# Kernel optimization log

Measured on AMD Instinct MI355X. Metric: run time of the kernel, lower is better.

## Reference

```python
import jax, jax.numpy as jnp
import numpy as np

N, DIM = 100000, 512
HID = DIM // 2


def _mlp(z, W1, b1, W2, b2):
    # shared scorer: [N, dim] -> [N, 1]
    h = jax.nn.relu(z @ W1 + b1)
    return h @ W2 + b2


def setup_inputs() -> dict:
    key = jax.random.key(0)
    k1, k2, k3, k4 = jax.random.split(key, 4)
    s1 = 1.0 / np.sqrt(DIM)
    s2 = 1.0 / np.sqrt(HID)
    return {
        "z1": jax.random.normal(k1, (N, DIM), dtype=jnp.float32),
        "z2": jax.random.normal(k2, (N, DIM), dtype=jnp.float32),
        "W1": jax.random.normal(k3, (DIM, HID), dtype=jnp.float32) * s1,
        "b1": jnp.zeros((HID,), dtype=jnp.float32),
        "W2": jax.random.normal(k4, (HID, 1), dtype=jnp.float32) * s2,
        "b2": jnp.zeros((1,), dtype=jnp.float32),
    }


def reference(z1, z2, W1, b1, W2, b2):
    x = _mlp(z1, W1, b1, W2, b2)  # [N, 1]
    y = _mlp(z2, W1, b1, W2, b2)  # [N, 1]
    # exp-normalize pair: score_x = e^x / (e^x + e^y) == sigmoid(x - y)
    # computed exactly as in the original (plain exp, no max-subtract)
    e_x = jnp.exp(x)
    e_y = jnp.exp(y)
    denom = e_x + e_y
    score_x = e_x / denom  # [N, 1]
    score_y = e_y / denom  # [N, 1]
    # diag(score) @ z  ==  score * z  (row-wise broadcast scale)
    return score_x * z1 + score_y * z2
```

## Files before the change

### kernel.cpp

```cpp
#include <hip/hip_runtime.h>
#include <hip/hip_bf16.h>
#include <cmath>

#define DIM 512
#define HID 256
#define ROWS_PB 32
#define NCHUNK 16
#define CB 16384

typedef __attribute__((ext_vector_type(8))) short short8;
typedef __attribute__((ext_vector_type(4))) float f32x4;

__device__ __forceinline__ unsigned short f2bf(float f) {
  union { float f; unsigned u; } v; v.f = f;
  unsigned u = v.u;
  return (unsigned short)((u + 0x7FFFu + ((u >> 16) & 1u)) >> 16);
}

__global__ void w1_swz_kernel(const float* __restrict__ W1,
                              unsigned short* __restrict__ w1s) {
  int tid = blockIdx.x * blockDim.x + threadIdx.x;
  if (tid >= DIM * HID) return;
  int k = tid / HID;
  int c = tid - k * HID;
  w1s[(((k >> 3) * HID) + c) * 8 + (k & 7)] = f2bf(W1[tid]);
}

__device__ __forceinline__ short8 cvt8(const f32x4 p0, const f32x4 p1) {
  short8 r;
  r[0] = (short)f2bf(p0[0]); r[1] = (short)f2bf(p0[1]);
  r[2] = (short)f2bf(p0[2]); r[3] = (short)f2bf(p0[3]);
  r[4] = (short)f2bf(p1[0]); r[5] = (short)f2bf(p1[1]);
  r[6] = (short)f2bf(p1[2]); r[7] = (short)f2bf(p1[3]);
  return r;
}

__global__ __launch_bounds__(256, 4) void fa_main_kernel(
    const float* __restrict__ z1, const float* __restrict__ z2,
    const unsigned short* __restrict__ w1s,
    const float* __restrict__ b1, const float* __restrict__ W2,
    const float* __restrict__ b2, float* __restrict__ out, int n) {
  __shared__ unsigned short Bs[2][CB / 2];
  __shared__ float xs[2][ROWS_PB];

  const int t = threadIdx.x;
  const int w = t >> 6;
  const int l = t & 63;
  const int l15 = l & 15, l16 = l >> 4;
  const int src = w & 1;
  const int tile = w >> 1;
  const int row0 = blockIdx.x * ROWS_PB;
  if (row0 >= n) return;
  const int myrow = row0 + tile * 16 + l15;
  const bool rok = myrow < n;
  const float* zz = src ? z2 : z1;
  const float* ap = zz + (size_t)myrow * DIM + (l16 << 3);
  const f32x4 zf4 = (f32x4){0.f, 0.f, 0.f, 0.f};

  {
    const char* gsrc = (const char*)w1s + l * 16;
#pragma unroll
    for (int r = w; r < 16; r += 4)
      __builtin_amdgcn_global_load_lds(
          (const __attribute__((address_space(1))) void*)(gsrc + r * 1024),
          (__attribute__((address_space(3))) void*)((char*)&Bs[0][0] + r * 1024),
          16, 0, 0);
  }
  f32x4 pa0 = rok ? *(const f32x4*)(ap) : zf4;
  f32x4 pa1 = rok ? *(const f32x4*)(ap + 4) : zf4;

  f32x4 acc[16];
#pragma unroll
  for (int f = 0; f < 16; ++f) acc[f] = zf4;

  __syncthreads();

  for (int c = 0; c < NCHUNK; ++c) {
    const int cur = c & 1;
    f32x4 na0 = zf4, na1 = zf4;
    if (c + 1 < NCHUNK) {
      const char* gsrc = (const char*)w1s + (c + 1) * CB + l * 16;
#pragma unroll
      for (int r = w; r < 16; r += 4)
        __builtin_amdgcn_global_load_lds(
            (const __attribute__((address_space(1))) void*)(gsrc + r * 1024),
            (__attribute__((address_space(3))) void*)((char*)&Bs[cur ^ 1][0] +
                                                      r * 1024),
            16, 0, 0);
      const float* apn = ap + ((c + 1) << 5);
      na0 = rok ? *(const f32x4*)(apn) : zf4;
      na1 = rok ? *(const f32x4*)(apn + 4) : zf4;
    }
    const short8 af = cvt8(pa0, pa1);
    const short8* bp = (const short8*)&Bs[cur][0] + (l16 << 8) + l15;
#pragma unroll
    for (int f = 0; f < 16; ++f) {
      const short8 bf = bp[f << 4];
      acc[f] = __builtin_amdgcn_mfma_f32_16x16x32_bf16(af, bf, acc[f], 0, 0, 0);
    }
    pa0 = na0;
    pa1 = na1;
    __syncthreads();
  }

  float part[4] = {0.f, 0.f, 0.f, 0.f};
#pragma unroll
  for (int f = 0; f < 16; ++f) {
    const int cc = (f << 4) + l15;
    const float w2v = W2[cc];
    const float b1v = b1[cc];
#pragma unroll
    for (int r = 0; r < 4; ++r) {
      const float h = acc[f][r] + b1v;
      part[r] += (h > 0.f) ? h * w2v : 0.f;
    }
  }
#pragma unroll
  for (int r = 0; r < 4; ++r) {
#pragma unroll
    for (int m = 1; m < 16; m <<= 1) part[r] += __shfl_xor(part[r], m, 16);
  }
  if (l15 == 0) {
#pragma unroll
    for (int r = 0; r < 4; ++r)
      xs[src][tile * 16 + (l16 << 2) + r] = part[r];
  }
  __syncthreads();

  const int colh = src << 8;
#pragma unroll 1
  for (int r = 0; r < 16; ++r) {
    const int rl = tile * 16 + r;
    const int grow = row0 + rl;
    if (grow < n) {
      const float d = xs[1][rl] - xs[0][rl];
      const float sx = 1.f / (1.f + __expf(d));
      const float sy = 1.f - sx;
      const size_t off = (size_t)grow * DIM + colh + (l << 2);
      const f32x4 a4 = *(const f32x4*)(z1 + off);
      const f32x4 b4 = *(const f32x4*)(z2 + off);
      f32x4 o;
      o[0] = sx * a4[0] + sy * b4[0];
      o[1] = sx * a4[1] + sy * b4[1];
      o[2] = sx * a4[2] + sy * b4[2];
      o[3] = sx * a4[3] + sy * b4[3];
      *(f32x4*)(out + off) = o;
    }
  }
}

extern "C" void kernel_launch(void* const* d_in, const int* in_sizes, int n_in,
                              void* d_out, int out_size, void* d_ws,
                              size_t ws_size, hipStream_t stream) {
  const float* z1 = (const float*)d_in[0];
  const float* z2 = (const float*)d_in[1];
  const float* W1 = (const float*)d_in[2];
  const float* b1 = (const float*)d_in[3];
  const float* W2 = (const float*)d_in[4];
  const float* b2 = (const float*)d_in[5];
  float* out = (float*)d_out;
  const int n = in_sizes[0] / DIM;
  unsigned short* w1s = (unsigned short*)d_ws;

  hipLaunchKernelGGL(w1_swz_kernel, dim3((DIM * HID + 255) / 256), dim3(256),
                     0, stream, W1, w1s);
  const int nwg = (n + ROWS_PB - 1) / ROWS_PB;
  hipLaunchKernelGGL(fa_main_kernel, dim3(nwg), dim3(256), 0, stream, z1, z2,
                     w1s, b1, W2, b2, out, n);
}
```

Baseline: 211.8 us.

## Deepen A-prefetch and replace per-chunk syncthreads with explicit vmcnt waits

Restructures the K-chunk loop so W1 staging into LDS is issued after a single barrier per iteration. The barrier is guarded by a hand-written s_waitcnt vmcnt that waits only for the current chunk's LDS loads. A-operand register prefetch now runs two chunks ahead using a double-buffered register array. The loop is fully unrolled and fenced with sched_barriers. The aim is to hide more global-load latency and drop the trailing __syncthreads, at the cost of more registers and a dependence on exact memory-op counts.

```diff
diff --git a/kernel.cpp b/kernel.cpp
--- a/kernel.cpp
+++ b/kernel.cpp
@@ -50,57 +50,61 @@
   const int src = w & 1;
   const int tile = w >> 1;
   const int row0 = blockIdx.x * ROWS_PB;
-  if (row0 >= n) return;
   const int myrow = row0 + tile * 16 + l15;
   const bool rok = myrow < n;
   const float* zz = src ? z2 : z1;
   const float* ap = zz + (size_t)myrow * DIM + (l16 << 3);
   const f32x4 zf4 = (f32x4){0.f, 0.f, 0.f, 0.f};
 
-  {
-    const char* gsrc = (const char*)w1s + l * 16;
+  auto STAGE = [&](int cc) {
+    const char* gsrc = (const char*)w1s + cc * CB + l * 16;
+    char* ldst = (char*)&Bs[cc & 1][0];
 #pragma unroll
-    for (int r = w; r < 16; r += 4)
+    for (int r = 0; r < 4; ++r) {
+      const int rr = w + r * 4;
       __builtin_amdgcn_global_load_lds(
-          (const __attribute__((address_space(1))) void*)(gsrc + r * 1024),
-          (__attribute__((address_space(3))) void*)((char*)&Bs[0][0] + r * 1024),
-          16, 0, 0);
-  }
-  f32x4 pa0 = rok ? *(const f32x4*)(ap) : zf4;
-  f32x4 pa1 = rok ? *(const f32x4*)(ap + 4) : zf4;
+          (const __attribute__((address_space(1))) void*)(gsrc + rr * 1024),
+          (__attribute__((address_space(3))) void*)(ldst + rr * 1024), 16, 0,
+          0);
+    }
+  };
+
+  f32x4 pa[2][2];
+  STAGE(0);
+  __builtin_amdgcn_sched_barrier(0);
+  pa[0][0] = rok ? *(const f32x4*)(ap) : zf4;
+  pa[0][1] = rok ? *(const f32x4*)(ap + 4) : zf4;
+  pa[1][0] = rok ? *(const f32x4*)(ap + 32) : zf4;
+  pa[1][1] = rok ? *(const f32x4*)(ap + 36) : zf4;
+  __builtin_amdgcn_sched_barrier(0);
 
   f32x4 acc[16];
 #pragma unroll
   for (int f = 0; f < 16; ++f) acc[f] = zf4;
 
-  __syncthreads();
-
+#pragma unroll
   for (int c = 0; c < NCHUNK; ++c) {
-    const int cur = c & 1;
-    f32x4 na0 = zf4, na1 = zf4;
-    if (c + 1 < NCHUNK) {
-      const char* gsrc = (const char*)w1s + (c + 1) * CB + l * 16;
-#pragma unroll
-      for (int r = w; r < 16; r += 4)
-        __builtin_amdgcn_global_load_lds(
-            (const __attribute__((address_space(1))) void*)(gsrc + r * 1024),
-            (__attribute__((address_space(3))) void*)((char*)&Bs[cur ^ 1][0] +
-                                                      r * 1024),
-            16, 0, 0);
-      const float* apn = ap + ((c + 1) << 5);
-      na0 = rok ? *(const f32x4*)(apn) : zf4;
-      na1 = rok ? *(const f32x4*)(apn + 4) : zf4;
+    if (c < NCHUNK - 1)
+      asm volatile("s_waitcnt vmcnt(2)" ::: "memory");
+    else
+      asm volatile("s_waitcnt vmcnt(0)" ::: "memory");
+    __builtin_amdgcn_s_barrier();
+    __builtin_amdgcn_sched_barrier(0);
+    if (c + 1 < NCHUNK) STAGE(c + 1);
+    __builtin_amdgcn_sched_barrier(0);
+    const short8 af = cvt8(pa[c & 1][0], pa[c & 1][1]);
+    if (c + 2 < NCHUNK) {
+      const float* apn = ap + ((c + 2) << 5);
+      pa[c & 1][0] = rok ? *(const f32x4*)(apn) : zf4;
+      pa[c & 1][1] = rok ? *(const f32x4*)(apn + 4) : zf4;
     }
-    const short8 af = cvt8(pa0, pa1);
-    const short8* bp = (const short8*)&Bs[cur][0] + (l16 << 8) + l15;
+    __builtin_amdgcn_sched_barrier(0);
+    const short8* bp = (const short8*)&Bs[c & 1][0] + (l16 << 8) + l15;
 #pragma unroll
     for (int f = 0; f < 16; ++f) {
       const short8 bf = bp[f << 4];
       acc[f] = __builtin_amdgcn_mfma_f32_16x16x32_bf16(af, bf, acc[f], 0, 0, 0);
     }
-    pa0 = na0;
-    pa1 = na1;
-    __syncthreads();
   }
 
   float part[4] = {0.f, 0.f, 0.f, 0.f};
```

New measurement: 245.5 us. 15.9% more time.

## Double row tile per block, stage W1 through registers, prefetch activations two chunks ahead

Applied to the files above, without the earlier changes.

Each block now covers 64 rows with 512 threads, so every W1 chunk staged in LDS is shared by twice as many rows. The async global-to-LDS loads are replaced by register loads that are written to the alternate LDS buffer after the MFMAs. Activation loads are prefetched two chunks ahead, and the chunk loop is fully unrolled with a scheduling barrier. The goal is to cut redundant W1 traffic and hide global latency, at the cost of more registers and occupancy limited to 2 blocks of 512 threads.

```diff
diff --git a/kernel.cpp b/kernel.cpp
--- a/kernel.cpp
+++ b/kernel.cpp
@@ -4,12 +4,13 @@
 
 #define DIM 512
 #define HID 256
-#define ROWS_PB 32
+#define ROWS_PB 64
 #define NCHUNK 16
 #define CB 16384
 
 typedef __attribute__((ext_vector_type(8))) short short8;
 typedef __attribute__((ext_vector_type(4))) float f32x4;
+typedef __attribute__((ext_vector_type(4))) unsigned int u32x4;
 
 __device__ __forceinline__ unsigned short f2bf(float f) {
   union { float f; unsigned u; } v; v.f = f;
@@ -35,39 +36,48 @@
   return r;
 }
 
-__global__ __launch_bounds__(256, 4) void fa_main_kernel(
+__global__ __launch_bounds__(512, 2) void fa_main_kernel(
     const float* __restrict__ z1, const float* __restrict__ z2,
     const unsigned short* __restrict__ w1s,
-    const float* __restrict__ b1, const float* __restrict__ W2,
-    const float* __restrict__ b2, float* __restrict__ out, int n) {
-  __shared__ unsigned short Bs[2][CB / 2];
+    const float* __restrict__ bias1, const float* __restrict__ W2,
+    const float* __restrict__ bias2, float* __restrict__ out, int n) {
+  __shared__ char Bbuf[2][CB];
   __shared__ float xs[2][ROWS_PB];
 
   const int t = threadIdx.x;
   const int w = t >> 6;
   const int l = t & 63;
   const int l15 = l & 15, l16 = l >> 4;
-  const int src = w & 1;
+  const int s = w & 1;
   const int tile = w >> 1;
   const int row0 = blockIdx.x * ROWS_PB;
-  if (row0 >= n) return;
   const int myrow = row0 + tile * 16 + l15;
   const bool rok = myrow < n;
-  const float* zz = src ? z2 : z1;
+  const float* zz = s ? z2 : z1;
   const float* ap = zz + (size_t)myrow * DIM + (l16 << 3);
   const f32x4 zf4 = (f32x4){0.f, 0.f, 0.f, 0.f};
 
-  {
-    const char* gsrc = (const char*)w1s + l * 16;
-#pragma unroll
-    for (int r = w; r < 16; r += 4)
-      __builtin_amdgcn_global_load_lds(
-          (const __attribute__((address_space(1))) void*)(gsrc + r * 1024),
-          (__attribute__((address_space(3))) void*)((char*)&Bs[0][0] + r * 1024),
-          16, 0, 0);
+  u32x4 breg0, breg1;
+#define BLOAD(c)                                              \
+  {                                                           \
+    const u32x4* g = (const u32x4*)w1s + (c) * 1024 + l;      \
+    breg0 = g[w * 64];                                        \
+    breg1 = g[(w + 8) * 64];                                  \
   }
-  f32x4 pa0 = rok ? *(const f32x4*)(ap) : zf4;
-  f32x4 pa1 = rok ? *(const f32x4*)(ap + 4) : zf4;
+#define BWRITE(c)                                             \
+  {                                                           \
+    u32x4* d = (u32x4*)&Bbuf[(c) & 1][0] + l;                 \
+    d[w * 64] = breg0;                                        \
+    d[(w + 8) * 64] = breg1;                                  \
+  }
+
+  BLOAD(0);
+  f32x4 pa0[2], pa1[2];
+  pa0[0] = rok ? *(const f32x4*)(ap) : zf4;
+  pa0[1] = rok ? *(const f32x4*)(ap + 4) : zf4;
+  pa1[0] = rok ? *(const f32x4*)(ap + 32) : zf4;
+  pa1[1] = rok ? *(const f32x4*)(ap + 36) : zf4;
+  BWRITE(0);
 
   f32x4 acc[16];
 #pragma unroll
@@ -75,31 +85,31 @@
 
   __syncthreads();
 
+#pragma unroll
   for (int c = 0; c < NCHUNK; ++c) {
-    const int cur = c & 1;
-    f32x4 na0 = zf4, na1 = zf4;
-    if (c + 1 < NCHUNK) {
-      const char* gsrc = (const char*)w1s + (c + 1) * CB + l * 16;
-#pragma unroll
-      for (int r = w; r < 16; r += 4)
-        __builtin_amdgcn_global_load_lds(
-            (const __attribute__((address_space(1))) void*)(gsrc + r * 1024),
-            (__attribute__((address_space(3))) void*)((char*)&Bs[cur ^ 1][0] +
-                                                      r * 1024),
-            16, 0, 0);
-      const float* apn = ap + ((c + 1) << 5);
-      na0 = rok ? *(const f32x4*)(apn) : zf4;
-      na1 = rok ? *(const f32x4*)(apn + 4) : zf4;
+    const short8 af =
+        (c & 1) ? cvt8(pa1[0], pa1[1]) : cvt8(pa0[0], pa0[1]);
+    if (c + 1 < NCHUNK) BLOAD(c + 1);
+    if (c + 2 < NCHUNK) {
+      const float* apn = ap + ((c + 2) << 5);
+      if (c & 1) {
+        pa1[0] = rok ? *(const f32x4*)(apn) : zf4;
+        pa1[1] = rok ? *(const f32x4*)(apn + 4) : zf4;
+      } else {
+        pa0[0] = rok ? *(const f32x4*)(apn) : zf4;
+        pa0[1] = rok ? *(const f32x4*)(apn + 4) : zf4;
+      }
     }
-    const short8 af = cvt8(pa0, pa1);
-    const short8* bp = (const short8*)&Bs[cur][0] + (l16 << 8) + l15;
+    __builtin_amdgcn_sched_barrier(0);
+    const short8* bp =
+        (const short8*)&Bbuf[c & 1][0] + (l16 << 8) + l15;
 #pragma unroll
     for (int f = 0; f < 16; ++f) {
       const short8 bf = bp[f << 4];
-      acc[f] = __builtin_amdgcn_mfma_f32_16x16x32_bf16(af, bf, acc[f], 0, 0, 0);
+      acc[f] =
+          __builtin_amdgcn_mfma_f32_16x16x32_bf16(af, bf, acc[f], 0, 0, 0);
     }
-    pa0 = na0;
-    pa1 = na1;
+    if (c + 1 < NCHUNK) BWRITE(c + 1);
     __syncthreads();
   }
 
@@ -108,11 +118,11 @@
   for (int f = 0; f < 16; ++f) {
     const int cc = (f << 4) + l15;
     const float w2v = W2[cc];
-    const float b1v = b1[cc];
+    const float b1v = bias1[cc];
 #pragma unroll
     for (int r = 0; r < 4; ++r) {
-      const float h = acc[f][r] + b1v;
-      part[r] += (h > 0.f) ? h * w2v : 0.f;
+      const float hh = acc[f][r] + b1v;
+      part[r] += (hh > 0.f) ? hh * w2v : 0.f;
     }
   }
 #pragma unroll
@@ -123,18 +133,19 @@
   if (l15 == 0) {
 #pragma unroll
     for (int r = 0; r < 4; ++r)
-      xs[src][tile * 16 + (l16 << 2) + r] = part[r];
+      xs[s][tile * 16 + (l16 << 2) + r] = part[r];
   }
   __syncthreads();
 
-  const int colh = src << 8;
-#pragma unroll 1
+  const int colh = s << 8;
+#pragma unroll 2
   for (int r = 0; r < 16; ++r) {
     const int rl = tile * 16 + r;
     const int grow = row0 + rl;
     if (grow < n) {
-      const float d = xs[1][rl] - xs[0][rl];
-      const float sx = 1.f / (1.f + __expf(d));
+      const float x = xs[0][rl];
+      const float y = xs[1][rl];
+      const float sx = 1.f / (1.f + __expf(y - x));
       const float sy = 1.f - sx;
       const size_t off = (size_t)grow * DIM + colh + (l << 2);
       const f32x4 a4 = *(const f32x4*)(z1 + off);
@@ -147,6 +158,8 @@
       *(f32x4*)(out + off) = o;
     }
   }
+#undef BLOAD
+#undef BWRITE
 }
 
 extern "C" void kernel_launch(void* const* d_in, const int* in_sizes, int n_in,
@@ -165,6 +178,6 @@
   hipLaunchKernelGGL(w1_swz_kernel, dim3((DIM * HID + 255) / 256), dim3(256),
                      0, stream, W1, w1s);
   const int nwg = (n + ROWS_PB - 1) / ROWS_PB;
-  hipLaunchKernelGGL(fa_main_kernel, dim3(nwg), dim3(256), 0, stream, z1, z2,
+  hipLaunchKernelGGL(fa_main_kernel, dim3(nwg), dim3(512), 0, stream, z1, z2,
                      w1s, b1, W2, b2, out, n);
 }
```

After: 274.9 us. 1.3x slower.
